# Kernel tuning notes

Hardware: AMD Instinct MI355X
Metric: run time of the kernel (lower is better)

Reference implementation:

```python
import jax, jax.numpy as jnp
import numpy as np

B, T, D, H = 4, 2048, 1024, 16
DH = D // H
T2 = T // 2
LN_EPS = 1e-5


def setup_inputs() -> dict:
    key = jax.random.key(0)
    ks = jax.random.split(key, 10)
    x = jax.random.normal(ks[0], (B, T, D), dtype=jnp.float32)
    query = jax.random.normal(ks[1], (1, 1, D), dtype=jnp.float32) * 0.02
    s = 1.0 / np.sqrt(D)
    Wk = jax.random.uniform(ks[2], (D, D), jnp.float32, -s, s)
    Wv = jax.random.uniform(ks[3], (D, D), jnp.float32, -s, s)
    Wt = jax.random.uniform(ks[4], (D, D // 2), jnp.float32, -s, s)
    bt = jax.random.uniform(ks[5], (D // 2,), jnp.float32, -s, s)
    Wm = jax.random.uniform(ks[6], (D, 1), jnp.float32, -s, s)
    bm = jax.random.uniform(ks[7], (1,), jnp.float32, -s, s)
    ln_g = jnp.ones((D,), jnp.float32)
    ln_b = jnp.zeros((D,), jnp.float32)
    return {"x": x, "query": query, "Wk": Wk, "Wv": Wv, "Wt": Wt,
            "bt": bt, "Wm": Wm, "bm": bm, "ln_g": ln_g, "ln_b": ln_b}


def reference(x, query, Wk, Wv, Wt, bt, Wm, bm, ln_g, ln_b):
    Bx, Tx, d = x.shape
    t2 = Tx // 2
    h, dh = H, DH
    # projections -> (B, T, H, dh)
    k = (x @ Wk).reshape(Bx, Tx, h, dh)
    v = (x @ Wv).reshape(Bx, Tx, h, dh)
    q = query.reshape(h, dh)  # single learned query, shared over all coarse positions
    # scores: (B, H, T) then broadcast to (B, H, T2, T) with position-dependent mask t > 2j
    scores = jnp.einsum('hd,bthd->bht', q, k) / jnp.sqrt(jnp.asarray(dh, x.dtype))
    j_idx = jnp.arange(t2)[:, None]   # (T2, 1)
    t_idx = jnp.arange(Tx)[None, :]   # (1, T)
    mask_bias = jnp.where(t_idx > 2 * j_idx, -jnp.inf, 0.0).astype(x.dtype)  # (T2, T)
    attn = jax.nn.softmax(scores[:, :, None, :] + mask_bias[None, None], axis=-1)  # (B,H,T2,T)
    pooled = jnp.einsum('bhjt,bthd->bjhd', attn, v).reshape(Bx, t2, d)  # (B, T2, d)
    # LayerNorm over last dim
    mu = jnp.mean(pooled, axis=-1, keepdims=True)
    var = jnp.mean(jnp.square(pooled - mu), axis=-1, keepdims=True)
    pooled_n = (pooled - mu) * jax.lax.rsqrt(var + LN_EPS) * ln_g + ln_b
    theta = pooled_n @ Wt + bt                 # (B, T2, d//2)
    mag = jax.nn.sigmoid(pooled_n @ Wm + bm)   # (B, T2, 1)
    return theta, mag
```

## Files before the change

### kernel.cpp

```cpp
#include <hip/hip_runtime.h>
#include <hip/hip_bf16.h>
#include <cstdint>
#include <cstddef>

constexpr int Bc  = 4;
constexpr int Tc  = 2048;
constexpr int Dc  = 1024;
constexpr int Hc  = 16;
constexpr int DHc = 64;
constexpr int T2c = 1024;
constexpr int NCc = 32;
constexpr int NEXT = 1152;
#define LN_EPS_F 1e-5f

typedef __attribute__((ext_vector_type(8))) short bf16x8;
typedef __attribute__((ext_vector_type(8))) ushort ushort8_t;
typedef __attribute__((ext_vector_type(4))) float f32x4;

__device__ inline ushort f2bf(float f) {
    union { float f; uint32_t u; } v; v.f = f;
    uint32_t r = v.u + 0x7FFFu + ((v.u >> 16) & 1u);
    return (ushort)(r >> 16);
}
__device__ inline float bf2f(ushort u) {
    union { uint32_t u; float f; } v; v.u = ((uint32_t)u) << 16;
    return v.f;
}

__device__ inline void async_copy16(const void* g, void* lds) {
    __builtin_amdgcn_global_load_lds(
        (const __attribute__((address_space(1))) void*)g,
        (__attribute__((address_space(3))) void*)lds, 16, 0, 0);
}

constexpr int PREP_CVT  = 8192;
constexpr int PREP_WV   = PREP_CVT + 1024;
constexpr int PREP_WT   = PREP_WV + 512;
constexpr int PREP_QK   = PREP_WT + 64;
constexpr int PREP_ZERO = PREP_QK + 56;

__global__ __launch_bounds__(256) void k_prep(const float* __restrict__ x,
                                              const float* __restrict__ Wv,
                                              const float* __restrict__ Wt,
                                              const float* __restrict__ Wk,
                                              const float* __restrict__ query,
                                              ushort* __restrict__ xb,
                                              ushort* __restrict__ WvXT,
                                              ushort* __restrict__ WtT) {
    __shared__ float tile[32][33];
    int blk = blockIdx.x;
    int tid = threadIdx.x;
    if (blk < PREP_CVT) {
        int i = (blk * 256 + tid) * 4;
        float4 f = *(const float4*)(x + i);
        ushort4 o;
        o.x = f2bf(f.x); o.y = f2bf(f.y); o.z = f2bf(f.z); o.w = f2bf(f.w);
        *(ushort4*)(xb + i) = o;
    } else if (blk < PREP_WV) {
        int b2 = blk - PREP_CVT;
        int bx = b2 & 31, by = b2 >> 5;
        int tx = tid & 31, ty = tid >> 5;
        #pragma unroll
        for (int r = 0; r < 32; r += 8)
            tile[ty + r][tx] = Wv[(size_t)(by * 32 + ty + r) * Dc + bx * 32 + tx];
        __syncthreads();
        #pragma unroll
        for (int r = 0; r < 32; r += 8)
            WvXT[(size_t)(bx * 32 + ty + r) * Dc + by * 32 + tx] = f2bf(tile[tx][ty + r]);
    } else if (blk < PREP_WT) {
        int b2 = blk - PREP_WV;
        int bx = b2 & 15, by = b2 >> 4;
        int tx = tid & 31, ty = tid >> 5;
        #pragma unroll
        for (int r = 0; r < 32; r += 8)
            tile[ty + r][tx] = Wt[(size_t)(by * 32 + ty + r) * (Dc / 2) + bx * 32 + tx];
        __syncthreads();
        #pragma unroll
        for (int r = 0; r < 32; r += 8)
            WtT[(size_t)(bx * 32 + ty + r) * Dc + by * 32 + tx] = f2bf(tile[tx][ty + r]);
    } else if (blk < PREP_QK) {
        int idx = (blk - PREP_WT) * 256 + tid;
        int h = idx >> 10, i = idx & (Dc - 1);
        const float* wrow = Wk + (size_t)i * Dc + h * DHc;
        const float* qh   = query + h * DHc;
        float s = 0.f;
        #pragma unroll 8
        for (int d = 0; d < DHc; ++d) s += wrow[d] * qh[d];
        WvXT[(size_t)(Dc + h) * Dc + i] = f2bf(s * 0.125f);
    } else {
        int idx = (blk - PREP_QK) * 256 + tid;
        uint4 z = {0, 0, 0, 0};
        *(uint4*)(WvXT + (size_t)1040 * Dc + idx * 8) = z;
    }
}

__global__ __launch_bounds__(256) void k_gemm_v(const ushort* __restrict__ A,
                                                const ushort* __restrict__ Bt,
                                                ushort* __restrict__ v,
                                                float* __restrict__ scores) {
    constexpr int K = Dc;
    __shared__ ushort As[128 * 64];
    __shared__ ushort Bs[64 * 64];
    int tid = threadIdx.x;
    int wid = tid >> 6, lane = tid & 63;
    int tile_m = blockIdx.x * 128, tile_n = blockIdx.y * 64;
    int wm = wid >> 1, wn = wid & 1;

    f32x4 acc[4][2] = {};

    int lrow = lane >> 3;
    int lchunk = lane & 7;
    int schunk = lchunk ^ lrow;
    int quad = lane >> 4, l15 = lane & 15;
    int sw = l15 & 7;

    for (int k0 = 0; k0 < K; k0 += 64) {
        #pragma unroll
        for (int r = 0; r < 4; ++r) {
            int rowgrp = wid * 4 + r;
            int row = rowgrp * 8 + lrow;
            async_copy16(A + (size_t)(tile_m + row) * K + k0 + schunk * 8,
                         &As[rowgrp * 8 * 64]);
        }
        #pragma unroll
        for (int r = 0; r < 2; ++r) {
            int rowgrp = wid * 2 + r;
            int row = rowgrp * 8 + lrow;
            async_copy16(Bt + (size_t)(tile_n + row) * K + k0 + schunk * 8,
                         &Bs[rowgrp * 8 * 64]);
        }
        __syncthreads();

        bf16x8 a_frag[4][2], b_frag[2][2];
        #pragma unroll
        for (int s = 0; s < 2; ++s) {
            int gc = s * 4 + quad;
            #pragma unroll
            for (int i = 0; i < 4; ++i)
                a_frag[i][s] = *(const bf16x8*)&As[(wm * 64 + i * 16 + l15) * 64 + ((gc ^ sw) * 8)];
            #pragma unroll
            for (int j = 0; j < 2; ++j)
                b_frag[j][s] = *(const bf16x8*)&Bs[(wn * 32 + j * 16 + l15) * 64 + ((gc ^ sw) * 8)];
        }
        #pragma unroll
        for (int s = 0; s < 2; ++s)
            #pragma unroll
            for (int i = 0; i < 4; ++i)
                #pragma unroll
                for (int j = 0; j < 2; ++j)
                    acc[i][j] = __builtin_amdgcn_mfma_f32_16x16x32_bf16(
                        a_frag[i][s], b_frag[j][s], acc[i][j], 0, 0, 0);
        __syncthreads();
    }

    #pragma unroll
    for (int j = 0; j < 2; ++j) {
        int col = tile_n + wn * 32 + j * 16 + l15;
        #pragma unroll
        for (int i = 0; i < 4; ++i) {
            #pragma unroll
            for (int r = 0; r < 4; ++r) {
                int row = tile_m + wm * 64 + i * 16 + quad * 4 + r;
                float val = acc[i][j][r];
                if (col < Dc) {
                    v[(size_t)row * Dc + col] = f2bf(val);
                } else if (col < Dc + Hc) {
                    int h = col - Dc;
                    int b2 = row >> 11, t = row & (Tc - 1);
                    scores[((size_t)b2 * Hc + h) * Tc + t] = val;
                }
            }
        }
    }
}

__global__ __launch_bounds__(256) void k_gemm_t(const ushort* __restrict__ A,
                                                const ushort* __restrict__ Bt,
                                                const float* __restrict__ bias,
                                                float* __restrict__ C,
                                                int N, int K) {
    __shared__ ushort As[64 * 64];
    __shared__ ushort Bs[64 * 64];
    int tid = threadIdx.x;
    int wid = tid >> 6, lane = tid & 63;
    int tile_m = blockIdx.x * 64, tile_n = blockIdx.y * 64;
    int wm = wid >> 1, wn = wid & 1;

    f32x4 acc[2][2] = {};

    int lrow = lane >> 3;
    int lchunk = lane & 7;
    int schunk = lchunk ^ lrow;
    int quad = lane >> 4, l15 = lane & 15;
    int sw = l15 & 7;

    for (int k0 = 0; k0 < K; k0 += 64) {
        #pragma unroll
        for (int r = 0; r < 2; ++r) {
            int rowgrp = wid * 2 + r;
            int row = rowgrp * 8 + lrow;
            async_copy16(A + (size_t)(tile_m + row) * K + k0 + schunk * 8,
                         &As[rowgrp * 8 * 64]);
            async_copy16(Bt + (size_t)(tile_n + row) * K + k0 + schunk * 8,
                         &Bs[rowgrp * 8 * 64]);
        }
        __syncthreads();

        bf16x8 a_frag[2][2], b_frag[2][2];
        #pragma unroll
        for (int s = 0; s < 2; ++s) {
            int gc = s * 4 + quad;
            #pragma unroll
            for (int i = 0; i < 2; ++i)
                a_frag[i][s] = *(const bf16x8*)&As[(wm * 32 + i * 16 + l15) * 64 + ((gc ^ sw) * 8)];
            #pragma unroll
            for (int j = 0; j < 2; ++j)
                b_frag[j][s] = *(const bf16x8*)&Bs[(wn * 32 + j * 16 + l15) * 64 + ((gc ^ sw) * 8)];
        }
        #pragma unroll
        for (int s = 0; s < 2; ++s)
            #pragma unroll
            for (int i = 0; i < 2; ++i)
                #pragma unroll
                for (int j = 0; j < 2; ++j)
                    acc[i][j] = __builtin_amdgcn_mfma_f32_16x16x32_bf16(
                        a_frag[i][s], b_frag[j][s], acc[i][j], 0, 0, 0);
        __syncthreads();
    }

    #pragma unroll
    for (int j = 0; j < 2; ++j) {
        int col = tile_n + wn * 32 + j * 16 + l15;
        float bv = bias[col];
        #pragma unroll
        for (int i = 0; i < 2; ++i) {
            #pragma unroll
            for (int r = 0; r < 4; ++r) {
                int row = tile_m + wm * 32 + i * 16 + quad * 4 + r;
                C[(size_t)row * N + col] = acc[i][j][r] + bv;
            }
        }
    }
}

__global__ __launch_bounds__(64) void k_chunk(const float* __restrict__ scores,
                                              const ushort* __restrict__ v,
                                              float* __restrict__ chunkL,
                                              float* __restrict__ chunkAcc) {
    int idx = blockIdx.x;
    int c = idx & (NCc - 1);
    int bh = idx / NCc;
    int h = bh & (Hc - 1), b = bh / Hc;
    int lane = threadIdx.x;
    int tgrp = lane >> 3;
    int dgrp = lane & 7;
    int t0 = c * 64;
    const float* srow = scores + (size_t)bh * Tc + t0;
    const ushort* vbase = v + ((size_t)b * Tc + t0) * Dc + h * DHc + dgrp * 8;
    float acc[8] = {};
    float lsum = 0.f;
    #pragma unroll
    for (int it = 0; it < 8; ++it) {
        int t = it * 8 + tgrp;
        float e = expf(srow[t]);
        ushort8_t vv = *(const ushort8_t*)(vbase + (size_t)t * Dc);
        #pragma unroll
        for (int k = 0; k < 8; ++k) acc[k] += e * bf2f(vv[k]);
        lsum += e;
    }
    #pragma unroll
    for (int m = 8; m < 64; m <<= 1) {
        #pragma unroll
        for (int k = 0; k < 8; ++k) acc[k] += __shfl_xor(acc[k], m);
        lsum += __shfl_xor(lsum, m);
    }
    if (tgrp == 0) {
        float4 lo = {acc[0], acc[1], acc[2], acc[3]};
        float4 hi = {acc[4], acc[5], acc[6], acc[7]};
        *(float4*)&chunkAcc[(size_t)idx * DHc + dgrp * 8]     = lo;
        *(float4*)&chunkAcc[(size_t)idx * DHc + dgrp * 8 + 4] = hi;
        if (dgrp == 0) chunkL[idx] = lsum;
    }
}

__global__ __launch_bounds__(64) void k_emit(const float* __restrict__ scores,
                                             const ushort* __restrict__ v,
                                             const float* __restrict__ chunkL,
                                             const float* __restrict__ chunkAcc,
                                             ushort* __restrict__ pooled) {
    int idx = blockIdx.x;
    int c = idx & (NCc - 1);
    int bh = idx / NCc;
    int h = bh & (Hc - 1), b = bh / Hc;
    int lane = threadIdx.x;
    int tgrp = lane >> 3, dgrp = lane & 7;
    int t0 = c * 64;
    __shared__ float E[64];
    __shared__ ushort vs[64 * DHc];
    E[lane] = expf(scores[(size_t)bh * Tc + t0 + lane]);
    const ushort* vbase = v + ((size_t)b * Tc + t0) * Dc + h * DHc + dgrp * 8;
    #pragma unroll
    for (int it = 0; it < 8; ++it) {
        int t = it * 8 + tgrp;
        *(ushort8_t*)&vs[t * DHc + dgrp * 8] = *(const ushort8_t*)(vbase + (size_t)t * Dc);
    }
    float acc = 0.f;
    for (int cc = 0; cc < c; ++cc)
        acc += chunkAcc[((size_t)bh * NCc + cc) * DHc + lane];
    float lP = (lane < c) ? chunkL[bh * NCc + lane] : 0.f;
    #pragma unroll
    for (int m = 1; m < 64; m <<= 1) lP += __shfl_xor(lP, m);
    float l = lP;
    __syncthreads();
    #pragma unroll 4
    for (int t = 0; t < 64; t += 2) {
        float e = E[t];
        acc += e * bf2f(vs[t * DHc + lane]);
        l += e;
        int j = (t0 + t) >> 1;
        pooled[((size_t)b * T2c + j) * Dc + h * DHc + lane] = f2bf(acc / l);
        float e2 = E[t + 1];
        acc += e2 * bf2f(vs[(t + 1) * DHc + lane]);
        l += e2;
    }
}

__global__ __launch_bounds__(256) void k_lnmag(const ushort* __restrict__ pooled,
                                               const float* __restrict__ g,
                                               const float* __restrict__ be,
                                               const float* __restrict__ Wm,
                                               const float* __restrict__ bm,
                                               ushort* __restrict__ out,
                                               float* __restrict__ mag) {
    int row = blockIdx.x;
    const ushort* p = pooled + (size_t)row * Dc;
    int tid = threadIdx.x;
    __shared__ float red[256];
    __shared__ float mu_s, rstd_s;
    float x4[4];
    {
        ushort4 u = *(const ushort4*)(p + tid * 4);
        x4[0] = bf2f(u.x); x4[1] = bf2f(u.y); x4[2] = bf2f(u.z); x4[3] = bf2f(u.w);
    }
    red[tid] = x4[0] + x4[1] + x4[2] + x4[3];
    __syncthreads();
    for (int off = 128; off > 0; off >>= 1) {
        if (tid < off) red[tid] += red[tid + off];
        __syncthreads();
    }
    if (tid == 0) mu_s = red[0] * (1.f / Dc);
    __syncthreads();
    float mu = mu_s;
    float vs = 0.f;
    #pragma unroll
    for (int k = 0; k < 4; ++k) { float d = x4[k] - mu; vs += d * d; }
    red[tid] = vs;
    __syncthreads();
    for (int off = 128; off > 0; off >>= 1) {
        if (tid < off) red[tid] += red[tid + off];
        __syncthreads();
    }
    if (tid == 0) rstd_s = rsqrtf(red[0] * (1.f / Dc) + LN_EPS_F);
    __syncthreads();
    float rstd = rstd_s;
    int i = tid * 4;
    float4 gv = *(const float4*)(g + i);
    float4 bv = *(const float4*)(be + i);
    float4 wv = *(const float4*)(Wm + i);
    float n0 = (x4[0] - mu) * rstd * gv.x + bv.x;
    float n1 = (x4[1] - mu) * rstd * gv.y + bv.y;
    float n2 = (x4[2] - mu) * rstd * gv.z + bv.z;
    float n3 = (x4[3] - mu) * rstd * gv.w + bv.w;
    ushort4 o;
    o.x = f2bf(n0); o.y = f2bf(n1); o.z = f2bf(n2); o.w = f2bf(n3);
    *(ushort4*)(out + (size_t)row * Dc + i) = o;
    red[tid] = bf2f(o.x) * wv.x + bf2f(o.y) * wv.y + bf2f(o.z) * wv.z + bf2f(o.w) * wv.w;
    __syncthreads();
    for (int off = 128; off > 0; off >>= 1) {
        if (tid < off) red[tid] += red[tid + off];
        __syncthreads();
    }
    if (tid == 0) {
        float z = red[0] + bm[0];
        mag[row] = 1.f / (1.f + expf(-z));
    }
}

extern "C" void kernel_launch(void* const* d_in, const int* in_sizes, int n_in,
                              void* d_out, int out_size, void* d_ws, size_t ws_size,
                              hipStream_t stream) {
    const float* x     = (const float*)d_in[0];
    const float* query = (const float*)d_in[1];
    const float* Wk    = (const float*)d_in[2];
    const float* Wv    = (const float*)d_in[3];
    const float* Wt    = (const float*)d_in[4];
    const float* bt    = (const float*)d_in[5];
    const float* Wm    = (const float*)d_in[6];
    const float* bm    = (const float*)d_in[7];
    const float* ln_g  = (const float*)d_in[8];
    const float* ln_b  = (const float*)d_in[9];
    float* out = (float*)d_out;

    char* w = (char*)d_ws;
    auto alloc = [&](size_t bytes) { char* p = w; w += (bytes + 255) & ~(size_t)255; return p; };
    ushort* v        = (ushort*)alloc((size_t)Bc * Tc * Dc * 2);
    ushort* pooled   = (ushort*)alloc((size_t)Bc * T2c * Dc * 2);
    ushort* xb       = (ushort*)alloc((size_t)Bc * Tc * Dc * 2);
    ushort* pooledn  = (ushort*)alloc((size_t)Bc * T2c * Dc * 2);
    ushort* WvXT     = (ushort*)alloc((size_t)NEXT * Dc * 2);
    ushort* WtT      = (ushort*)alloc((size_t)(Dc / 2) * Dc * 2);
    float*  scores   = (float*) alloc((size_t)Bc * Hc * Tc * 4);
    float*  chunkL   = (float*) alloc((size_t)Bc * Hc * NCc * 4);
    float*  chunkAcc = (float*) alloc((size_t)Bc * Hc * NCc * DHc * 4);

    k_prep<<<PREP_ZERO, 256, 0, stream>>>(x, Wv, Wt, Wk, query, xb, WvXT, WtT);
    k_gemm_v<<<dim3((Bc * Tc) / 128, 17), 256, 0, stream>>>(xb, WvXT, v, scores);
    k_chunk<<<Bc * Hc * NCc, 64, 0, stream>>>(scores, v, chunkL, chunkAcc);
    k_emit<<<Bc * Hc * NCc, 64, 0, stream>>>(scores, v, chunkL, chunkAcc, pooled);
    k_lnmag<<<Bc * T2c, 256, 0, stream>>>(pooled, ln_g, ln_b, Wm, bm, pooledn,
                                          out + (size_t)Bc * T2c * (Dc / 2));
    k_gemm_t<<<dim3((Bc * T2c) / 64, (Dc / 2) / 64), 256, 0, stream>>>(
        pooledn, WtT, bt, out, Dc / 2, Dc);
}
```

Before: 177.6 us.

## Fuse LayerNorm and magnitude head into emit; enlarge GEMM tiles

The separate LayerNorm/sigmoid kernel is removed. Its work now runs in k_emit: a per-(batch, chunk) atomic counter picks the last of the 16 head blocks to finish, and that block normalises its 32 rows with wave shuffles. The V/score GEMM tile grows to 128x128, using 9 column tiles instead of 17, and the theta GEMM tile grows to 128x64. Together these cut launch overhead and improve operand reuse. The cost is that the single 64-thread last block serialises the LayerNorm work for each chunk, and the larger tiles reduce grid size and occupancy.

Measured after the change: 275.8 us. +55.3%, slower.

```diff
diff --git a/kernel.cpp b/kernel.cpp
--- a/kernel.cpp
+++ b/kernel.cpp
@@ -38,6 +38,7 @@
 constexpr int PREP_WT   = PREP_WV + 512;
 constexpr int PREP_QK   = PREP_WT + 64;
 constexpr int PREP_ZERO = PREP_QK + 56;
+constexpr int PREP_TOT  = PREP_ZERO + 1;
 
 __global__ __launch_bounds__(256) void k_prep(const float* __restrict__ x,
                                               const float* __restrict__ Wv,
@@ -46,7 +47,8 @@
                                               const float* __restrict__ query,
                                               ushort* __restrict__ xb,
                                               ushort* __restrict__ WvXT,
-                                              ushort* __restrict__ WtT) {
+                                              ushort* __restrict__ WtT,
+                                              unsigned* __restrict__ cnt) {
     __shared__ float tile[32][33];
     int blk = blockIdx.x;
     int tid = threadIdx.x;
@@ -87,10 +89,12 @@
         #pragma unroll 8
         for (int d = 0; d < DHc; ++d) s += wrow[d] * qh[d];
         WvXT[(size_t)(Dc + h) * Dc + i] = f2bf(s * 0.125f);
-    } else {
+    } else if (blk < PREP_ZERO) {
         int idx = (blk - PREP_QK) * 256 + tid;
         uint4 z = {0, 0, 0, 0};
         *(uint4*)(WvXT + (size_t)1040 * Dc + idx * 8) = z;
+    } else {
+        if (tid < Bc * NCc) cnt[tid] = 0;
     }
 }
 
@@ -100,13 +104,13 @@
                                                 float* __restrict__ scores) {
     constexpr int K = Dc;
     __shared__ ushort As[128 * 64];
-    __shared__ ushort Bs[64 * 64];
+    __shared__ ushort Bs[128 * 64];
     int tid = threadIdx.x;
     int wid = tid >> 6, lane = tid & 63;
-    int tile_m = blockIdx.x * 128, tile_n = blockIdx.y * 64;
+    int tile_m = blockIdx.x * 128, tile_n = blockIdx.y * 128;
     int wm = wid >> 1, wn = wid & 1;
 
-    f32x4 acc[4][2] = {};
+    f32x4 acc[4][4] = {};
 
     int lrow = lane >> 3;
     int lchunk = lane & 7;
@@ -121,17 +125,12 @@
             int row = rowgrp * 8 + lrow;
             async_copy16(A + (size_t)(tile_m + row) * K + k0 + schunk * 8,
                          &As[rowgrp * 8 * 64]);
-        }
-        #pragma unroll
-        for (int r = 0; r < 2; ++r) {
-            int rowgrp = wid * 2 + r;
-            int row = rowgrp * 8 + lrow;
             async_copy16(Bt + (size_t)(tile_n + row) * K + k0 + schunk * 8,
                          &Bs[rowgrp * 8 * 64]);
         }
         __syncthreads();
 
-        bf16x8 a_frag[4][2], b_frag[2][2];
+        bf16x8 a_frag[4][2], b_frag[4][2];
         #pragma unroll
         for (int s = 0; s < 2; ++s) {
             int gc = s * 4 + quad;
@@ -139,23 +138,23 @@
             for (int i = 0; i < 4; ++i)
                 a_frag[i][s] = *(const bf16x8*)&As[(wm * 64 + i * 16 + l15) * 64 + ((gc ^ sw) * 8)];
             #pragma unroll
-            for (int j = 0; j < 2; ++j)
-                b_frag[j][s] = *(const bf16x8*)&Bs[(wn * 32 + j * 16 + l15) * 64 + ((gc ^ sw) * 8)];
+            for (int j = 0; j < 4; ++j)
+                b_frag[j][s] = *(const bf16x8*)&Bs[(wn * 64 + j * 16 + l15) * 64 + ((gc ^ sw) * 8)];
         }
         #pragma unroll
         for (int s = 0; s < 2; ++s)
             #pragma unroll
             for (int i = 0; i < 4; ++i)
                 #pragma unroll
-                for (int j = 0; j < 2; ++j)
+                for (int j = 0; j < 4; ++j)
                     acc[i][j] = __builtin_amdgcn_mfma_f32_16x16x32_bf16(
                         a_frag[i][s], b_frag[j][s], acc[i][j], 0, 0, 0);
         __syncthreads();
     }
 
     #pragma unroll
-    for (int j = 0; j < 2; ++j) {
-        int col = tile_n + wn * 32 + j * 16 + l15;
+    for (int j = 0; j < 4; ++j) {
+        int col = tile_n + wn * 64 + j * 16 + l15;
         #pragma unroll
         for (int i = 0; i < 4; ++i) {
             #pragma unroll
@@ -179,14 +178,14 @@
                                                 const float* __restrict__ bias,
                                                 float* __restrict__ C,
                                                 int N, int K) {
-    __shared__ ushort As[64 * 64];
+    __shared__ ushort As[128 * 64];
     __shared__ ushort Bs[64 * 64];
     int tid = threadIdx.x;
     int wid = tid >> 6, lane = tid & 63;
-    int tile_m = blockIdx.x * 64, tile_n = blockIdx.y * 64;
+    int tile_m = blockIdx.x * 128, tile_n = blockIdx.y * 64;
     int wm = wid >> 1, wn = wid & 1;
 
-    f32x4 acc[2][2] = {};
+    f32x4 acc[4][2] = {};
 
     int lrow = lane >> 3;
     int lchunk = lane & 7;
@@ -196,23 +195,28 @@
 
     for (int k0 = 0; k0 < K; k0 += 64) {
         #pragma unroll
+        for (int r = 0; r < 4; ++r) {
+            int rowgrp = wid * 4 + r;
+            int row = rowgrp * 8 + lrow;
+            async_copy16(A + (size_t)(tile_m + row) * K + k0 + schunk * 8,
+                         &As[rowgrp * 8 * 64]);
+        }
+        #pragma unroll
         for (int r = 0; r < 2; ++r) {
             int rowgrp = wid * 2 + r;
             int row = rowgrp * 8 + lrow;
-            async_copy16(A + (size_t)(tile_m + row) * K + k0 + schunk * 8,
-                         &As[rowgrp * 8 * 64]);
             async_copy16(Bt + (size_t)(tile_n + row) * K + k0 + schunk * 8,
                          &Bs[rowgrp * 8 * 64]);
         }
         __syncthreads();
 
-        bf16x8 a_frag[2][2], b_frag[2][2];
+        bf16x8 a_frag[4][2], b_frag[2][2];
         #pragma unroll
         for (int s = 0; s < 2; ++s) {
             int gc = s * 4 + quad;
             #pragma unroll
-            for (int i = 0; i < 2; ++i)
-                a_frag[i][s] = *(const bf16x8*)&As[(wm * 32 + i * 16 + l15) * 64 + ((gc ^ sw) * 8)];
+            for (int i = 0; i < 4; ++i)
+                a_frag[i][s] = *(const bf16x8*)&As[(wm * 64 + i * 16 + l15) * 64 + ((gc ^ sw) * 8)];
             #pragma unroll
             for (int j = 0; j < 2; ++j)
                 b_frag[j][s] = *(const bf16x8*)&Bs[(wn * 32 + j * 16 + l15) * 64 + ((gc ^ sw) * 8)];
@@ -220,7 +224,7 @@
         #pragma unroll
         for (int s = 0; s < 2; ++s)
             #pragma unroll
-            for (int i = 0; i < 2; ++i)
+            for (int i = 0; i < 4; ++i)
                 #pragma unroll
                 for (int j = 0; j < 2; ++j)
                     acc[i][j] = __builtin_amdgcn_mfma_f32_16x16x32_bf16(
@@ -233,10 +237,10 @@
         int col = tile_n + wn * 32 + j * 16 + l15;
         float bv = bias[col];
         #pragma unroll
-        for (int i = 0; i < 2; ++i) {
+        for (int i = 0; i < 4; ++i) {
             #pragma unroll
             for (int r = 0; r < 4; ++r) {
-                int row = tile_m + wm * 32 + i * 16 + quad * 4 + r;
+                int row = tile_m + wm * 64 + i * 16 + quad * 4 + r;
                 C[(size_t)row * N + col] = acc[i][j][r] + bv;
             }
         }
@@ -287,7 +291,14 @@
                                              const ushort* __restrict__ v,
                                              const float* __restrict__ chunkL,
                                              const float* __restrict__ chunkAcc,
-                                             ushort* __restrict__ pooled) {
+                                             const float* __restrict__ g,
+                                             const float* __restrict__ be,
+                                             const float* __restrict__ Wm,
+                                             const float* __restrict__ bm,
+                                             ushort* __restrict__ pooled,
+                                             ushort* __restrict__ pooledn,
+                                             float* __restrict__ mag,
+                                             unsigned* __restrict__ cnt) {
     int idx = blockIdx.x;
     int c = idx & (NCc - 1);
     int bh = idx / NCc;
@@ -323,66 +334,62 @@
         acc += e2 * bf2f(vs[(t + 1) * DHc + lane]);
         l += e2;
     }
-}
-
-__global__ __launch_bounds__(256) void k_lnmag(const ushort* __restrict__ pooled,
-                                               const float* __restrict__ g,
-                                               const float* __restrict__ be,
-                                               const float* __restrict__ Wm,
-                                               const float* __restrict__ bm,
-                                               ushort* __restrict__ out,
-                                               float* __restrict__ mag) {
-    int row = blockIdx.x;
-    const ushort* p = pooled + (size_t)row * Dc;
-    int tid = threadIdx.x;
-    __shared__ float red[256];
-    __shared__ float mu_s, rstd_s;
-    float x4[4];
-    {
-        ushort4 u = *(const ushort4*)(p + tid * 4);
-        x4[0] = bf2f(u.x); x4[1] = bf2f(u.y); x4[2] = bf2f(u.z); x4[3] = bf2f(u.w);
-    }
-    red[tid] = x4[0] + x4[1] + x4[2] + x4[3];
+
+    __threadfence();
+    __shared__ unsigned last_s;
+    if (lane == 0) last_s = atomicAdd(&cnt[b * NCc + c], 1u);
     __syncthreads();
-    for (int off = 128; off > 0; off >>= 1) {
-        if (tid < off) red[tid] += red[tid + off];
-        __syncthreads();
-    }
-    if (tid == 0) mu_s = red[0] * (1.f / Dc);
-    __syncthreads();
-    float mu = mu_s;
-    float vs = 0.f;
-    #pragma unroll
-    for (int k = 0; k < 4; ++k) { float d = x4[k] - mu; vs += d * d; }
-    red[tid] = vs;
-    __syncthreads();
-    for (int off = 128; off > 0; off >>= 1) {
-        if (tid < off) red[tid] += red[tid + off];
-        __syncthreads();
-    }
-    if (tid == 0) rstd_s = rsqrtf(red[0] * (1.f / Dc) + LN_EPS_F);
-    __syncthreads();
-    float rstd = rstd_s;
-    int i = tid * 4;
-    float4 gv = *(const float4*)(g + i);
-    float4 bv = *(const float4*)(be + i);
-    float4 wv = *(const float4*)(Wm + i);
-    float n0 = (x4[0] - mu) * rstd * gv.x + bv.x;
-    float n1 = (x4[1] - mu) * rstd * gv.y + bv.y;
-    float n2 = (x4[2] - mu) * rstd * gv.z + bv.z;
-    float n3 = (x4[3] - mu) * rstd * gv.w + bv.w;
-    ushort4 o;
-    o.x = f2bf(n0); o.y = f2bf(n1); o.z = f2bf(n2); o.w = f2bf(n3);
-    *(ushort4*)(out + (size_t)row * Dc + i) = o;
-    red[tid] = bf2f(o.x) * wv.x + bf2f(o.y) * wv.y + bf2f(o.z) * wv.z + bf2f(o.w) * wv.w;
-    __syncthreads();
-    for (int off = 128; off > 0; off >>= 1) {
-        if (tid < off) red[tid] += red[tid + off];
-        __syncthreads();
-    }
-    if (tid == 0) {
-        float z = red[0] + bm[0];
-        mag[row] = 1.f / (1.f + expf(-z));
+    if (last_s != Hc - 1) return;
+    __threadfence();
+
+    int i0 = lane * 16;
+    float gv[16], bev[16], wmv[16];
+    #pragma unroll
+    for (int q = 0; q < 16; q += 4) {
+        float4 t1 = *(const float4*)(g + i0 + q);
+        gv[q] = t1.x; gv[q+1] = t1.y; gv[q+2] = t1.z; gv[q+3] = t1.w;
+        float4 t2 = *(const float4*)(be + i0 + q);
+        bev[q] = t2.x; bev[q+1] = t2.y; bev[q+2] = t2.z; bev[q+3] = t2.w;
+        float4 t3 = *(const float4*)(Wm + i0 + q);
+        wmv[q] = t3.x; wmv[q+1] = t3.y; wmv[q+2] = t3.z; wmv[q+3] = t3.w;
+    }
+    float bmv = bm[0];
+    for (int jj = 0; jj < 32; ++jj) {
+        int row = b * T2c + c * 32 + jj;
+        const ushort* prow = pooled + (size_t)row * Dc + i0;
+        float x[16];
+        float s = 0.f;
+        #pragma unroll
+        for (int q = 0; q < 16; q += 4) {
+            ushort4 u = *(const ushort4*)(prow + q);
+            x[q] = bf2f(u.x); x[q+1] = bf2f(u.y); x[q+2] = bf2f(u.z); x[q+3] = bf2f(u.w);
+            s += x[q] + x[q+1] + x[q+2] + x[q+3];
+        }
+        #pragma unroll
+        for (int m = 1; m < 64; m <<= 1) s += __shfl_xor(s, m);
+        float mu = s * (1.f / Dc);
+        float vsum = 0.f;
+        #pragma unroll
+        for (int q = 0; q < 16; ++q) { float d = x[q] - mu; vsum += d * d; }
+        #pragma unroll
+        for (int m = 1; m < 64; m <<= 1) vsum += __shfl_xor(vsum, m);
+        float rstd = rsqrtf(vsum * (1.f / Dc) + LN_EPS_F);
+        float mdot = 0.f;
+        ushort o[16];
+        #pragma unroll
+        for (int q = 0; q < 16; ++q) {
+            float n = (x[q] - mu) * rstd * gv[q] + bev[q];
+            o[q] = f2bf(n);
+            mdot += bf2f(o[q]) * wmv[q];
+        }
+        #pragma unroll
+        for (int q = 0; q < 16; q += 4) {
+            ushort4 uo; uo.x = o[q]; uo.y = o[q+1]; uo.z = o[q+2]; uo.w = o[q+3];
+            *(ushort4*)(pooledn + (size_t)row * Dc + i0 + q) = uo;
+        }
+        #pragma unroll
+        for (int m = 1; m < 64; m <<= 1) mdot += __shfl_xor(mdot, m);
+        if (lane == 0) mag[row] = 1.f / (1.f + expf(-mdot - bmv));
     }
 }
 
@@ -403,22 +410,24 @@
 
     char* w = (char*)d_ws;
     auto alloc = [&](size_t bytes) { char* p = w; w += (bytes + 255) & ~(size_t)255; return p; };
-    ushort* v        = (ushort*)alloc((size_t)Bc * Tc * Dc * 2);
-    ushort* pooled   = (ushort*)alloc((size_t)Bc * T2c * Dc * 2);
-    ushort* xb       = (ushort*)alloc((size_t)Bc * Tc * Dc * 2);
-    ushort* pooledn  = (ushort*)alloc((size_t)Bc * T2c * Dc * 2);
-    ushort* WvXT     = (ushort*)alloc((size_t)NEXT * Dc * 2);
-    ushort* WtT      = (ushort*)alloc((size_t)(Dc / 2) * Dc * 2);
-    float*  scores   = (float*) alloc((size_t)Bc * Hc * Tc * 4);
-    float*  chunkL   = (float*) alloc((size_t)Bc * Hc * NCc * 4);
-    float*  chunkAcc = (float*) alloc((size_t)Bc * Hc * NCc * DHc * 4);
-
-    k_prep<<<PREP_ZERO, 256, 0, stream>>>(x, Wv, Wt, Wk, query, xb, WvXT, WtT);
-    k_gemm_v<<<dim3((Bc * Tc) / 128, 17), 256, 0, stream>>>(xb, WvXT, v, scores);
+    ushort*   v        = (ushort*)  alloc((size_t)Bc * Tc * Dc * 2);
+    ushort*   pooled   = (ushort*)  alloc((size_t)Bc * T2c * Dc * 2);
+    ushort*   xb       = (ushort*)  alloc((size_t)Bc * Tc * Dc * 2);
+    ushort*   pooledn  = (ushort*)  alloc((size_t)Bc * T2c * Dc * 2);
+    ushort*   WvXT     = (ushort*)  alloc((size_t)NEXT * Dc * 2);
+    ushort*   WtT      = (ushort*)  alloc((size_t)(Dc / 2) * Dc * 2);
+    float*    scores   = (float*)   alloc((size_t)Bc * Hc * Tc * 4);
+    float*    chunkL   = (float*)   alloc((size_t)Bc * Hc * NCc * 4);
+    float*    chunkAcc = (float*)   alloc((size_t)Bc * Hc * NCc * DHc * 4);
+    unsigned* cnt      = (unsigned*)alloc((size_t)Bc * NCc * 4);
+
+    k_prep<<<PREP_TOT, 256, 0, stream>>>(x, Wv, Wt, Wk, query, xb, WvXT, WtT, cnt);
+    k_gemm_v<<<dim3((Bc * Tc) / 128, NEXT / 128), 256, 0, stream>>>(xb, WvXT, v, scores);
     k_chunk<<<Bc * Hc * NCc, 64, 0, stream>>>(scores, v, chunkL, chunkAcc);
-    k_emit<<<Bc * Hc * NCc, 64, 0, stream>>>(scores, v, chunkL, chunkAcc, pooled);
-    k_lnmag<<<Bc * T2c, 256, 0, stream>>>(pooled, ln_g, ln_b, Wm, bm, pooledn,
-                                          out + (size_t)Bc * T2c * (Dc / 2));
-    k_gemm_t<<<dim3((Bc * T2c) / 64, (Dc / 2) / 64), 256, 0, stream>>>(
+    k_emit<<<Bc * Hc * NCc, 64, 0, stream>>>(scores, v, chunkL, chunkAcc,
+                                             ln_g, ln_b, Wm, bm,
+                                             pooled, pooledn,
+                                             out + (size_t)Bc * T2c * (Dc / 2), cnt);
+    k_gemm_t<<<dim3((Bc * T2c) / 128, (Dc / 2) / 64), 256, 0, stream>>>(
         pooledn, WtT, bt, out, Dc / 2, Dc);
 }
```
